# Kernel optimization log

Hardware: AMD Instinct MI355X
Metric: run time of the kernel (lower is better)

## Reference

```python
import jax, jax.numpy as jnp
import numpy as np

EPSILON = 1e-05
B, H, P, T, D = 256, 8, 64, 3, 64

def setup_inputs() -> dict:
    key = jax.random.key(0)
    ks = jax.random.split(key, 7)
    return {
        "X": jax.random.normal(ks[0], (B, H, P, T), dtype=jnp.float32),
        "W_left": jax.random.normal(ks[1], (H, P, D), dtype=jnp.float32),
        "W_right": jax.random.normal(ks[2], (H, P, D), dtype=jnp.float32),
        "fc1_w": jax.random.normal(ks[3], (D, H * P * D), dtype=jnp.float32) / np.sqrt(H * P * D),
        "fc1_b": jax.random.normal(ks[4], (D,), dtype=jnp.float32) * 0.01,
        "fc2_w": jax.random.normal(ks[5], (1, D), dtype=jnp.float32) / np.sqrt(D),
        "fc2_b": jax.random.normal(ks[6], (1,), dtype=jnp.float32) * 0.01,
    }

def reference(X, W_left, W_right, fc1_w, fc1_b, fc2_w, fc2_b):
    # pairwise deltas: [B,h,i,j,t]
    delta = X[..., :, None, :] - X[..., None, :, :]
    # relu(delta^2) is a no-op mathematically but kept faithful
    distance = jnp.sqrt(jnp.maximum(delta * delta, 0.0) + EPSILON)
    dX = (delta / distance) * jnp.exp(-distance)  # direction * exp(-dist)
    Xl = jnp.einsum('nhijt,hjd->nhidt', dX, W_left)
    Xr = jnp.einsum('nhijt,hjd->nhidt', dX, W_right)
    att = jnp.einsum('nhidt,nhidt->nhid', Xl, Xr)  # reduce over t
    flat = att.reshape(att.shape[0], -1)  # [B, h*p*d]
    hdn = jax.nn.silu(flat @ fc1_w.T + fc1_b)
    return hdn @ fc2_w.T + fc2_b  # [B, 1]
```

## Files before the change

kernel.cpp:

```cpp
#include <hip/hip_runtime.h>
#include <hip/hip_bf16.h>


typedef __attribute__((ext_vector_type(8))) short short8;
typedef __attribute__((ext_vector_type(4))) float f32x4;
typedef __attribute__((ext_vector_type(4))) unsigned short u16x4;

#define PADW 72
#define PADM 2056
#define KTOT 32768L

__device__ __forceinline__ unsigned short f2b(float x) {
  union { float f; unsigned int u; } v; v.f = x;
  return (unsigned short)((v.u + 0x7FFFu + ((v.u >> 16) & 1u)) >> 16);
}

__device__ __forceinline__ unsigned int pk_bf16(float lo, float hi) {
  unsigned int r;
  asm("v_cvt_pk_bf16_f32 %0, %1, %2" : "=v"(r) : "v"(lo), "v"(hi));
  return r;
}

__global__ __launch_bounds__(256)
void k_cvt_w(const float* __restrict__ in, unsigned short* __restrict__ out) {
  const int i = (blockIdx.x * 256 + threadIdx.x) * 4;
  f32x4 v = *(const f32x4*)(in + i);
  u16x4 o;
#pragma unroll
  for (int e = 0; e < 4; ++e) o[e] = f2b(v[e]);
  *(u16x4*)(out + i) = o;
}

__global__ __launch_bounds__(512, 1)
void k_fused(const float* __restrict__ X, const float* __restrict__ Wl_g,
             const float* __restrict__ Wr_g,
             const unsigned short* __restrict__ w1b,
             float* __restrict__ partial) {
  __shared__ float xs[16][3][64];
  __shared__ __align__(16) union {
    struct {
      unsigned short wl[64][PADW];
      unsigned short wr[64][PADW];
      unsigned short dxs[2][3][32][PADW];
    } a;
    float red[8][16][64];
  } u;
  __shared__ __align__(16) unsigned short att_s[16][PADM];

  const int blk  = blockIdx.x;
  const int ih   = blk & 1;
  const int h    = (blk >> 1) & 7;
  const int ng   = blk >> 4;
  const int tid  = threadIdx.x;
  const int lane = tid & 63;
  const int w    = tid >> 6;
  const int c0   = lane & 15;
  const int ks   = lane >> 4;
  const int iw   = (w >> 1) & 1;
  const int dw   = w & 1;
  const int qsub = w >> 2;

  const float* wlg = Wl_g + h * 4096;
  const float* wrg = Wr_g + h * 4096;
#pragma unroll
  for (int r = 0; r < 8; ++r) {
    int e = tid + r * 512;
    int j = e >> 6, d = e & 63;
    u.a.wl[d][j] = f2b(wlg[e]);
    u.a.wr[d][j] = f2b(wrg[e]);
  }
  {
    const long xbase = ((long)(ng * 16) * 8 + h) * 192;
#pragma unroll
    for (int r = 0; r < 6; ++r) {
      int e = tid + r * 512;
      int q = e / 192;
      int rem = e - q * 192;
      int i = rem / 3;
      int t = rem - i * 3;
      xs[q][t][i] = X[xbase + (long)q * 1536 + rem];
    }
  }
  __syncthreads();

  short8 bl[2][2], br[2][2];
#pragma unroll
  for (int cb = 0; cb < 2; ++cb)
#pragma unroll
    for (int kb = 0; kb < 2; ++kb) {
      const int d = c0 + 16 * cb + 32 * dw;
      const int j0 = ks * 8 + 32 * kb;
      bl[cb][kb] = *(const short8*)&u.a.wl[d][j0];
      br[cb][kb] = *(const short8*)&u.a.wr[d][j0];
    }

  const int dq  = tid >> 8;
  const int il  = (tid >> 3) & 31;
  const int jb  = (tid & 7) << 3;

  for (int it = 0; it < 8; ++it) {
    const int qd = it * 2 + dq;
    if (it) __syncthreads();
#pragma unroll
    for (int t = 0; t < 3; ++t) {
      const float xi = xs[qd][t][ih * 32 + il];
#pragma unroll
      for (int jj = 0; jj < 8; jj += 2) {
        float d0 = xi - xs[qd][t][jb + jj];
        float d1 = xi - xs[qd][t][jb + jj + 1];
        float s0 = d0 * d0 + 1e-5f;
        float s1 = d1 * d1 + 1e-5f;
        float i0 = rsqrtf(s0), i1 = rsqrtf(s1);
        float e0 = __expf(-(s0 * i0));
        float e1 = __expf(-(s1 * i1));
        *(unsigned int*)&u.a.dxs[dq][t][il][jb + jj] =
            pk_bf16(d0 * i0 * e0, d1 * i1 * e1);
      }
    }
    __syncthreads();

    const int q = it * 2 + qsub;
    f32x4 acc[2];
#pragma unroll
    for (int cb = 0; cb < 2; ++cb) {
      acc[cb][0] = 0.f; acc[cb][1] = 0.f; acc[cb][2] = 0.f; acc[cb][3] = 0.f;
    }
#pragma unroll
    for (int t = 0; t < 3; ++t) {
      short8 a0 = *(const short8*)&u.a.dxs[qsub][t][iw * 16 + c0][ks * 8];
      short8 a1 = *(const short8*)&u.a.dxs[qsub][t][iw * 16 + c0][ks * 8 + 32];
#pragma unroll
      for (int cb = 0; cb < 2; ++cb) {
        f32x4 xl; xl[0]=0.f; xl[1]=0.f; xl[2]=0.f; xl[3]=0.f;
        f32x4 xr; xr[0]=0.f; xr[1]=0.f; xr[2]=0.f; xr[3]=0.f;
        xl = __builtin_amdgcn_mfma_f32_16x16x32_bf16(a0, bl[cb][0], xl, 0, 0, 0);
        xl = __builtin_amdgcn_mfma_f32_16x16x32_bf16(a1, bl[cb][1], xl, 0, 0, 0);
        xr = __builtin_amdgcn_mfma_f32_16x16x32_bf16(a0, br[cb][0], xr, 0, 0, 0);
        xr = __builtin_amdgcn_mfma_f32_16x16x32_bf16(a1, br[cb][1], xr, 0, 0, 0);
        acc[cb] += xl * xr;
      }
    }
#pragma unroll
    for (int cb = 0; cb < 2; ++cb)
#pragma unroll
      for (int r = 0; r < 4; ++r) {
        int ro = iw * 16 + ks * 4 + r;
        int d = c0 + 16 * cb + 32 * dw;
        att_s[q][ro * 64 + d] = f2b(acc[cb][r]);
      }
  }
  __syncthreads();

  f32x4 facc[4];
#pragma unroll
  for (int cb = 0; cb < 4; ++cb) {
    facc[cb][0] = 0.f; facc[cb][1] = 0.f; facc[cb][2] = 0.f; facc[cb][3] = 0.f;
  }
  const unsigned short* bp =
      w1b + (long)c0 * KTOT + h * 4096 + ih * 2048 + w * 256 + ks * 8;
  const unsigned short* ap = &att_s[0][0] + c0 * PADM + w * 256 + ks * 8;
#pragma unroll
  for (int s = 0; s < 8; ++s) {
    short8 a = *(const short8*)(ap + s * 32);
#pragma unroll
    for (int cb = 0; cb < 4; ++cb) {
      short8 b = *(const short8*)(bp + (long)cb * 16 * KTOT + s * 32);
      facc[cb] = __builtin_amdgcn_mfma_f32_16x16x32_bf16(a, b, facc[cb], 0, 0, 0);
    }
  }
  __syncthreads();
#pragma unroll
  for (int cb = 0; cb < 4; ++cb)
#pragma unroll
    for (int r = 0; r < 4; ++r)
      u.red[w][ks * 4 + r][c0 + 16 * cb] = facc[cb][r];
  __syncthreads();
#pragma unroll
  for (int rep = 0; rep < 2; ++rep) {
    int e = tid + rep * 512;
    int nl = e >> 6, k = e & 63;
    float s = 0.f;
#pragma unroll
    for (int ww = 0; ww < 8; ++ww) s += u.red[ww][nl][k];
    partial[(((long)h * 2 + ih) * 256 + ng * 16 + nl) * 64 + k] = s;
  }
}

__global__ __launch_bounds__(256)
void k_fc2(const float* __restrict__ partial, const float* __restrict__ fc1_b,
           const float* __restrict__ fc2_w, const float* __restrict__ fc2_b,
           float* __restrict__ out) {
  const int tid = threadIdx.x;
  const int n = blockIdx.x * 4 + (tid >> 6);
  const int k = tid & 63;
  float s = fc1_b[k];
#pragma unroll
  for (int sp = 0; sp < 16; ++sp)
    s += partial[((long)sp * 256 + n) * 64 + k];
  float g = s / (1.f + __expf(-s));
  float v = g * fc2_w[k];
#pragma unroll
  for (int off = 32; off > 0; off >>= 1)
    v += __shfl_xor(v, off, 64);
  if (k == 0) out[n] = v + fc2_b[0];
}

extern "C" void kernel_launch(void* const* d_in, const int* in_sizes, int n_in,
                              void* d_out, int out_size, void* d_ws, size_t ws_size,
                              hipStream_t stream) {
  const float* X    = (const float*)d_in[0];
  const float* Wl   = (const float*)d_in[1];
  const float* Wr   = (const float*)d_in[2];
  const float* fc1w = (const float*)d_in[3];
  const float* fc1b = (const float*)d_in[4];
  const float* fc2w = (const float*)d_in[5];
  const float* fc2b = (const float*)d_in[6];
  float* out = (float*)d_out;

  char* ws = (char*)d_ws;
  unsigned short* w1b     = (unsigned short*)(ws);
  float*          partial = (float*)(ws + 4194304);

  hipLaunchKernelGGL(k_cvt_w, dim3(2048), dim3(256), 0, stream, fc1w, w1b);
  hipLaunchKernelGGL(k_fused, dim3(256), dim3(512), 0, stream, X, Wl, Wr, w1b, partial);
  hipLaunchKernelGGL(k_fc2,   dim3(64), dim3(256), 0, stream, partial, fc1b, fc2w, fc2b, out);
}
```

Before: 39.46 us.

## Merge conversion, fused, and fc2 kernels into one cooperative kernel with grid syncs

The three launches (fc1 weight bf16 conversion, fused attention+fc1, fc2 epilogue) become a single cooperative kernel. Each block converts a slice of fc1_w first, grid-syncs before the fc1 GEMM reads the bf16 weights, and grid-syncs again before 256 blocks each finish one batch row's silu and fc2. This removes launch gaps and inter-kernel drain, at the cost of two grid-wide barriers and a cooperative launch requirement. It also swaps rsqrtf/__expf for raw amdgcn rsq/exp2 builtins.

After: 98.21 us. 149% more time.

```diff
diff --git a/kernel.cpp b/kernel.cpp
--- a/kernel.cpp
+++ b/kernel.cpp
@@ -1,5 +1,8 @@
 #include <hip/hip_runtime.h>
 #include <hip/hip_bf16.h>
+#include <hip/hip_cooperative_groups.h>
+
+namespace cg = cooperative_groups;
 
 
 typedef __attribute__((ext_vector_type(8))) short short8;
@@ -21,21 +24,13 @@
   return r;
 }
 
-__global__ __launch_bounds__(256)
-void k_cvt_w(const float* __restrict__ in, unsigned short* __restrict__ out) {
-  const int i = (blockIdx.x * 256 + threadIdx.x) * 4;
-  f32x4 v = *(const f32x4*)(in + i);
-  u16x4 o;
-#pragma unroll
-  for (int e = 0; e < 4; ++e) o[e] = f2b(v[e]);
-  *(u16x4*)(out + i) = o;
-}
-
 __global__ __launch_bounds__(512, 1)
-void k_fused(const float* __restrict__ X, const float* __restrict__ Wl_g,
-             const float* __restrict__ Wr_g,
-             const unsigned short* __restrict__ w1b,
-             float* __restrict__ partial) {
+void k_all(const float* __restrict__ X, const float* __restrict__ Wl_g,
+           const float* __restrict__ Wr_g, const float* __restrict__ fc1w,
+           const float* __restrict__ fc1b, const float* __restrict__ fc2w,
+           const float* __restrict__ fc2b,
+           unsigned short* __restrict__ w1b, float* __restrict__ partial,
+           float* __restrict__ out) {
   __shared__ float xs[16][3][64];
   __shared__ __align__(16) union {
     struct {
@@ -60,6 +55,18 @@
   const int dw   = w & 1;
   const int qsub = w >> 2;
 
+  {
+    const int base = (blk * 512 + tid) * 16;
+#pragma unroll
+    for (int r = 0; r < 4; ++r) {
+      f32x4 v = *(const f32x4*)(fc1w + base + r * 4);
+      u16x4 o;
+#pragma unroll
+      for (int e = 0; e < 4; ++e) o[e] = f2b(v[e]);
+      *(u16x4*)(w1b + base + r * 4) = o;
+    }
+  }
+
   const float* wlg = Wl_g + h * 4096;
   const float* wrg = Wr_g + h * 4096;
 #pragma unroll
@@ -110,9 +117,10 @@
         float d1 = xi - xs[qd][t][jb + jj + 1];
         float s0 = d0 * d0 + 1e-5f;
         float s1 = d1 * d1 + 1e-5f;
-        float i0 = rsqrtf(s0), i1 = rsqrtf(s1);
-        float e0 = __expf(-(s0 * i0));
-        float e1 = __expf(-(s1 * i1));
+        float i0 = __builtin_amdgcn_rsqf(s0);
+        float i1 = __builtin_amdgcn_rsqf(s1);
+        float e0 = __builtin_amdgcn_exp2f(-1.44269504f * (s0 * i0));
+        float e1 = __builtin_amdgcn_exp2f(-1.44269504f * (s1 * i1));
         *(unsigned int*)&u.a.dxs[dq][t][il][jb + jj] =
             pk_bf16(d0 * i0 * e0, d1 * i1 * e1);
       }
@@ -151,6 +159,8 @@
   }
   __syncthreads();
 
+  cg::this_grid().sync();
+
   f32x4 facc[4];
 #pragma unroll
   for (int cb = 0; cb < 4; ++cb) {
@@ -184,25 +194,23 @@
     for (int ww = 0; ww < 8; ++ww) s += u.red[ww][nl][k];
     partial[(((long)h * 2 + ih) * 256 + ng * 16 + nl) * 64 + k] = s;
   }
-}
-
-__global__ __launch_bounds__(256)
-void k_fc2(const float* __restrict__ partial, const float* __restrict__ fc1_b,
-           const float* __restrict__ fc2_w, const float* __restrict__ fc2_b,
-           float* __restrict__ out) {
-  const int tid = threadIdx.x;
-  const int n = blockIdx.x * 4 + (tid >> 6);
-  const int k = tid & 63;
-  float s = fc1_b[k];
-#pragma unroll
-  for (int sp = 0; sp < 16; ++sp)
-    s += partial[((long)sp * 256 + n) * 64 + k];
-  float g = s / (1.f + __expf(-s));
-  float v = g * fc2_w[k];
-#pragma unroll
-  for (int off = 32; off > 0; off >>= 1)
-    v += __shfl_xor(v, off, 64);
-  if (k == 0) out[n] = v + fc2_b[0];
+
+  cg::this_grid().sync();
+
+  if (tid < 64) {
+    const int n = blk;
+    const int k = tid;
+    float s = fc1b[k];
+#pragma unroll
+    for (int sp = 0; sp < 16; ++sp)
+      s += partial[((long)sp * 256 + n) * 64 + k];
+    float g = s / (1.f + __expf(-s));
+    float v = g * fc2w[k];
+#pragma unroll
+    for (int off = 32; off > 0; off >>= 1)
+      v += __shfl_xor(v, off, 64);
+    if (k == 0) out[n] = v + fc2b[0];
+  }
 }
 
 extern "C" void kernel_launch(void* const* d_in, const int* in_sizes, int n_in,
@@ -221,7 +229,8 @@
   unsigned short* w1b     = (unsigned short*)(ws);
   float*          partial = (float*)(ws + 4194304);
 
-  hipLaunchKernelGGL(k_cvt_w, dim3(2048), dim3(256), 0, stream, fc1w, w1b);
-  hipLaunchKernelGGL(k_fused, dim3(256), dim3(512), 0, stream, X, Wl, Wr, w1b, partial);
-  hipLaunchKernelGGL(k_fc2,   dim3(64), dim3(256), 0, stream, partial, fc1b, fc2w, fc2b, out);
-}
+  void* args[] = {(void*)&X, (void*)&Wl, (void*)&Wr, (void*)&fc1w,
+                  (void*)&fc1b, (void*)&fc2w, (void*)&fc2b,
+                  (void*)&w1b, (void*)&partial, (void*)&out};
+  hipLaunchCooperativeKernel((void*)k_all, dim3(256), dim3(512), args, 0, stream);
+}
```
